# Performance work log

Hardware: AMD Instinct MI355X
Metric: run time of the kernel (lower is better)

Reference implementation:

```python
import jax, jax.numpy as jnp
import numpy as np

D = 32          # embedding_size
B = 16384       # batch_size
P = 16          # neighbor_sample_size (paths per item per hop)
NE = 100000     # n_entity
NU = 100000     # n_user
NR = 32         # n_relation
N_ITER = 2


def setup_inputs() -> dict:
    key = jax.random.key(0)
    ks = jax.random.split(key, 20)
    s = 0.1
    nrm = lambda k, sh: jax.random.normal(k, sh, dtype=jnp.float32) * s
    inp = {
        "user_table": nrm(ks[0], (NU, D)),
        "ent_table": nrm(ks[1], (NE, D)),
        "rel_table": nrm(ks[2], (NR, D)),
        # PyTorch LSTM params, gate order (i, f, g, o)
        "w_ih0": nrm(ks[3], (4 * D, 2 * D)),
        "w_hh0": nrm(ks[4], (4 * D, D)),
        "b_ih0": nrm(ks[5], (4 * D,)),
        "b_hh0": nrm(ks[6], (4 * D,)),
        "w_ih1": nrm(ks[7], (4 * D, 2 * D)),
        "w_hh1": nrm(ks[8], (4 * D, D)),
        "b_ih1": nrm(ks[9], (4 * D,)),
        "b_hh1": nrm(ks[10], (4 * D,)),
        "agg_w": nrm(ks[11], (D, D)),
        "agg_b": nrm(ks[12], (D,)),
        "users": jax.random.randint(ks[13], (B,), 0, NU),
        "items": jax.random.randint(ks[14], (B,), 0, NE),
        "ratings": jax.random.randint(ks[15], (B,), 0, 2),
        # hop h path table: [n_entity, P, 2*(h+1)+1]; values < 32 valid for both tables
        "lp0": jax.random.randint(ks[16], (NE, P, 3), 0, 32),
        "lp1": jax.random.randint(ks[17], (NE, P, 5), 0, 32),
    }
    return inp


def _lstm_last(seq, w_ih, w_hh, b_ih, b_hh):
    # seq: [N, T, 2D] -> final hidden state [N, D], PyTorch gate order i,f,g,o
    N = seq.shape[0]
    H = w_hh.shape[1]
    bias = b_ih + b_hh

    def step(carry, x):
        h, c = carry
        g = x @ w_ih.T + h @ w_hh.T + bias
        i, f, gg, o = jnp.split(g, 4, axis=-1)
        c = jax.nn.sigmoid(f) * c + jax.nn.sigmoid(i) * jnp.tanh(gg)
        h = jax.nn.sigmoid(o) * jnp.tanh(c)
        return (h, c), None

    h0 = jnp.zeros((N, H), seq.dtype)
    (h, _), _ = jax.lax.scan(step, (h0, h0), jnp.swapaxes(seq, 0, 1))
    return h


def _forward(user_table, ent_table, rel_table, lstm_params, agg_w, agg_b,
             users, items, ratings, lps):
    u = user_table[users]                # [B, D]
    items_emb = ent_table[items]         # [B, D]
    for hop in range(N_ITER):
        lp = lps[hop]
        w_ih, w_hh, b_ih, b_hh = lstm_params[hop]
        il = lp[items]                   # [B, P, 2*(hop+1)+1]
        seed_e = ent_table[il[:, :, 0]]  # [B, P, D]
        u_b = jnp.broadcast_to(u[:, None, :], seed_e.shape)
        first = jnp.concatenate([u_b, seed_e], -1)[:, :, None, :]   # [B,P,1,2D]
        rel_e = rel_table[il[:, :, 1::2]]                            # [B,P,hop+1,D]
        tail_e = ent_table[il[:, :, 2::2]]                           # [B,P,hop+1,D]
        rest = jnp.concatenate([rel_e, tail_e], -1)                  # [B,P,hop+1,2D]
        seq = jnp.concatenate([first, rest], 2).reshape(B * P, hop + 2, 2 * D)
        h = _lstm_last(seq, w_ih, w_hh, b_ih, b_hh)                  # [B*P, D]
        final = h.reshape(B, P, D).sum(axis=1)                       # hidden_out sum
        items_emb = (items_emb + final) @ agg_w.T + agg_b            # 'sum' aggregator
    scores = jnp.sum(u * items_emb, axis=-1)                         # [B]
    r = ratings.astype(scores.dtype)
    # stable BCE on sigmoid(scores)
    loss = -jnp.mean(r * jax.nn.log_sigmoid(scores) + (1.0 - r) * jax.nn.log_sigmoid(-scores))
    return loss, jax.nn.sigmoid(scores)


def reference(user_table, ent_table, rel_table,
              w_ih0, w_hh0, b_ih0, b_hh0,
              w_ih1, w_hh1, b_ih1, b_hh1,
              agg_w, agg_b,
              users, items, ratings, lp0, lp1):
    lstm_params = [(w_ih0, w_hh0, b_ih0, b_hh0), (w_ih1, w_hh1, b_ih1, b_hh1)]
    loss, scores_normalized = _forward(user_table, ent_table, rel_table,
                                       lstm_params, agg_w, agg_b,
                                       users, items, ratings, (lp0, lp1))
    return (loss, scores_normalized, items)
```

## Files before the change

### kernel.cpp

```cpp
#include <hip/hip_runtime.h>
#include <math.h>

#define D  32
#define BN 16384
#define PP 16

typedef __bf16 bf16x8 __attribute__((ext_vector_type(8)));
typedef __bf16 bf16x4 __attribute__((ext_vector_type(4)));
typedef float  floatx4 __attribute__((ext_vector_type(4)));

#define K1 1.44269504088896341f
#define K2 2.88539008177792681f

#define TR_OFF    0
#define TE_OFF    8448
#define BIAS_OFF  16896
#define WU_OFF    17408
#define WHH_OFF   27648
#define IMG_BYTES 37888
#define LDS_BYTES (IMG_BYTES + 8 * 1280)

__device__ __forceinline__ float sigf(float x) {
    float e = __builtin_amdgcn_exp2f(-x * K1);
    return __builtin_amdgcn_rcpf(1.0f + e);
}
__device__ __forceinline__ float logsigf(float x) {
    float ax = fabsf(x);
    float l = log1pf(__expf(-ax));
    return (x >= 0.0f) ? -l : x - l;
}
__device__ __forceinline__ floatx4 cvt4(bf16x4 v) {
    floatx4 r = { (float)v[0], (float)v[1], (float)v[2], (float)v[3] };
    return r;
}
__device__ __forceinline__ bf16x8 loadu8(const float* __restrict__ p) {
    float4 a = ((const float4*)p)[0], b = ((const float4*)p)[1];
    bf16x8 r = { (__bf16)a.x, (__bf16)a.y, (__bf16)a.z, (__bf16)a.w,
                 (__bf16)b.x, (__bf16)b.y, (__bf16)b.z, (__bf16)b.w };
    return r;
}

__global__ __launch_bounds__(256)
void prep_tables(const float* __restrict__ ent, const float* __restrict__ rel,
                 const float* __restrict__ wih0, const float* __restrict__ whh0,
                 const float* __restrict__ bih0, const float* __restrict__ bhh0,
                 const float* __restrict__ wih1, const float* __restrict__ whh1,
                 const float* __restrict__ bih1, const float* __restrict__ bhh1,
                 float* __restrict__ imgs_f)
{
    const int id = blockIdx.x * 256 + threadIdx.x;
    if (id < 16384) {
        const int hop = id >> 13;
        const int rest = id & 8191;
        const int tab = rest >> 12;
        const int k   = (rest >> 7) & 31;
        const int g   = rest & 127;
        const float* wih = hop ? wih1 : wih0;
        char* base = (char*)imgs_f + (size_t)hop * IMG_BYTES;
        if (tab == 0) {
            const float* w = wih + (size_t)g * 64;
            const float* s = rel + (size_t)k * 32;
            float a = (hop ? bih1[g] + bhh1[g] : bih0[g] + bhh0[g]);
            #pragma unroll
            for (int d = 0; d < 32; ++d) a = fmaf(w[d], s[d], a);
            *((__bf16*)(base + TR_OFF) + k * 132 + g) = (__bf16)a;
        } else {
            const float* w = wih + (size_t)g * 64 + 32;
            const float* s = ent + (size_t)k * 32;
            float a = 0.0f;
            #pragma unroll
            for (int d = 0; d < 32; ++d) a = fmaf(w[d], s[d], a);
            *((__bf16*)(base + TE_OFF) + k * 132 + g) = (__bf16)a;
        }
    } else if (id < 32768) {
        const int id2 = id - 16384;
        const int hop = id2 >> 13;
        const int rest = id2 & 8191;
        const int mat  = rest >> 12;
        const int e    = rest & 4095;
        const int gate = e >> 5, d = e & 31;
        char* base = (char*)imgs_f + (size_t)hop * IMG_BYTES;
        float v;
        if (mat == 0) v = (hop ? wih1 : wih0)[(size_t)gate * 64 + d];
        else          v = (hop ? whh1 : whh0)[(size_t)gate * 32 + d];
        *((__bf16*)(base + (mat ? WHH_OFF : WU_OFF)) + gate * 40 + d) = (__bf16)v;
    } else if (id < 33024) {
        const int id3 = id - 32768;
        const int hop = id3 >> 7;
        const int g   = id3 & 127;
        char* base = (char*)imgs_f + (size_t)hop * IMG_BYTES;
        ((float*)(base + BIAS_OFF))[g] = hop ? (bih1[g] + bhh1[g])
                                             : (bih0[g] + bhh0[g]);
    }
}

template<bool FIRST, bool LAST>
__device__ __forceinline__ void nonlin(
    floatx4* __restrict__ acc, float* __restrict__ cst,
    float* __restrict__ hlo, float* __restrict__ hhi,
    char* __restrict__ Hw, int q, int bnl)
{
    #pragma unroll
    for (int hf = 0; hf < 2; ++hf) {
        float* hout = hf ? hhi : hlo;
        #pragma unroll
        for (int r = 0; r < 4; ++r) {
            float gi = acc[0 + hf][r], gf = acc[2 + hf][r],
                  gg = acc[4 + hf][r], go = acc[6 + hf][r];
            float Ai = 1.0f + __builtin_amdgcn_exp2f(-gi * K1);
            float Af = 1.0f + __builtin_amdgcn_exp2f(-gf * K1);
            float G2 = __builtin_amdgcn_exp2f(gg * K2);
            float Gp = G2 + 1.0f, Gm = G2 - 1.0f;
            float cold = FIRST ? 0.0f : cst[hf * 4 + r];
            float num = cold * Ai * Gp + Gm * Af;
            float c = num * __builtin_amdgcn_rcpf(Af * Ai * Gp);
            cst[hf * 4 + r] = c;
            float Ao = 1.0f + __builtin_amdgcn_exp2f(-go * K1);
            float C2 = __builtin_amdgcn_exp2f(c * K2);
            hout[r] = (C2 - 1.0f) * __builtin_amdgcn_rcpf(Ao * (C2 + 1.0f));
        }
    }
    if (!LAST) {
        bf16x4 plo = { (__bf16)hlo[0], (__bf16)hlo[1], (__bf16)hlo[2], (__bf16)hlo[3] };
        bf16x4 phi = { (__bf16)hhi[0], (__bf16)hhi[1], (__bf16)hhi[2], (__bf16)hhi[3] };
        *(bf16x4*)(Hw + bnl * 80 + 8 * q)      = plo;
        *(bf16x4*)(Hw + bnl * 80 + 32 + 8 * q) = phi;
    }
}

__global__ __launch_bounds__(256, 3)
void hop_mfma(const float* __restrict__ user_table,
              const int*   __restrict__ users,
              const int*   __restrict__ items,
              const int*   __restrict__ lp0,
              const int*   __restrict__ lp1,
              const float* __restrict__ imgs_f,
              float* __restrict__ F0,
              float* __restrict__ F1)
{
    __shared__ __align__(16) char lds[LDS_BYTES];

    const bool second = blockIdx.x & 1;
    const int  idx    = blockIdx.x >> 1;
    const int tid  = threadIdx.x;
    const int lane = tid & 63;
    const int wave = tid >> 6;
    const int q    = lane >> 4;
    const int bnl  = lane & 15;

    {
        const float4* g = (const float4*)((const char*)imgs_f +
                                          (second ? IMG_BYTES : 0));
        float4* l = (float4*)lds;
        #pragma unroll
        for (int i = 0; i < 10; ++i) {
            int k = i * 256 + tid;
            if (k < IMG_BYTES / 16) l[k] = g[k];
        }
    }

    const char* Tr  = lds + TR_OFF;
    const char* Te  = lds + TE_OFF;
    const char* Wu  = lds + WU_OFF;
    const char* Whh = lds + WHH_OFF;
    char* HwA = lds + IMG_BYTES + (wave * 2 + 0) * 1280;
    char* HwB = lds + IMG_BYTES + (wave * 2 + 1) * 1280;

    const int fbA = idx * 8 + wave;
    const int fbB = fbA + 4;
    const int L   = second ? 5 : 3;
    const int* lp = second ? lp1 : lp0;
    const int* __restrict__ ilA = lp + ((size_t)items[fbA] * PP + bnl) * L;
    const int* __restrict__ ilB = lp + ((size_t)items[fbB] * PP + bnl) * L;

    bf16x8 buA = loadu8(user_table + (size_t)users[fbA] * D + q * 8);
    bf16x8 buB = loadu8(user_table + (size_t)users[fbB] * D + q * 8);

    __syncthreads();

    float cstA[8], cstB[8], hloA[4], hhiA[4], hloB[4], hhiB[4];

    {
        const int sA = ilA[0], sB = ilB[0];
        floatx4 accA[8], accB[8];
        #pragma unroll
        for (int mt = 0; mt < 8; ++mt) {
            const int go = 16 * mt + 4 * q;
            floatx4 bv = *(const floatx4*)(lds + BIAS_OFF + go * 4);
            accA[mt] = bv + cvt4(*(const bf16x4*)(Te + sA * 264 + go * 2));
            accB[mt] = bv + cvt4(*(const bf16x4*)(Te + sB * 264 + go * 2));
        }
        #pragma unroll
        for (int mt = 0; mt < 8; ++mt) {
            bf16x8 wu = *(const bf16x8*)(Wu + (16 * mt + bnl) * 80 + q * 16);
            accA[mt] = __builtin_amdgcn_mfma_f32_16x16x32_bf16(wu, buA, accA[mt], 0, 0, 0);
            accB[mt] = __builtin_amdgcn_mfma_f32_16x16x32_bf16(wu, buB, accB[mt], 0, 0, 0);
        }
        nonlin<true, false>(accA, cstA, hloA, hhiA, HwA, q, bnl);
        nonlin<true, false>(accB, cstB, hloB, hhiB, HwB, q, bnl);
    }

    #pragma unroll
    for (int t = 1; t < 3; ++t) {
        if (t == 2 && !second) break;
        const bool last = (t == (second ? 2 : 1));
        const int jA = ilA[2 * t - 1], kA = ilA[2 * t];
        const int jB = ilB[2 * t - 1], kB = ilB[2 * t];
        floatx4 accA[8], accB[8];
        #pragma unroll
        for (int mt = 0; mt < 8; ++mt) {
            const int go = 16 * mt + 4 * q;
            accA[mt] = cvt4(*(const bf16x4*)(Tr + jA * 264 + go * 2))
                     + cvt4(*(const bf16x4*)(Te + kA * 264 + go * 2));
            accB[mt] = cvt4(*(const bf16x4*)(Tr + jB * 264 + go * 2))
                     + cvt4(*(const bf16x4*)(Te + kB * 264 + go * 2));
        }
        bf16x8 bhA = *(const bf16x8*)(HwA + bnl * 80 + q * 16);
        bf16x8 bhB = *(const bf16x8*)(HwB + bnl * 80 + q * 16);
        #pragma unroll
        for (int mt = 0; mt < 8; ++mt) {
            bf16x8 wh = *(const bf16x8*)(Whh + (16 * mt + bnl) * 80 + q * 16);
            accA[mt] = __builtin_amdgcn_mfma_f32_16x16x32_bf16(wh, bhA, accA[mt], 0, 0, 0);
            accB[mt] = __builtin_amdgcn_mfma_f32_16x16x32_bf16(wh, bhB, accB[mt], 0, 0, 0);
        }
        if (last) {
            nonlin<false, true>(accA, cstA, hloA, hhiA, HwA, q, bnl);
            nonlin<false, true>(accB, cstB, hloB, hhiB, HwB, q, bnl);
        } else {
            nonlin<false, false>(accA, cstA, hloA, hhiA, HwA, q, bnl);
            nonlin<false, false>(accB, cstB, hloB, hhiB, HwB, q, bnl);
        }
    }

    #pragma unroll
    for (int r = 0; r < 4; ++r) {
        #pragma unroll
        for (int m = 1; m < 16; m <<= 1) {
            hloA[r] += __shfl_xor(hloA[r], m);
            hhiA[r] += __shfl_xor(hhiA[r], m);
            hloB[r] += __shfl_xor(hloB[r], m);
            hhiB[r] += __shfl_xor(hhiB[r], m);
        }
    }
    if (bnl == 0) {
        float* Fout = (second ? F1 : F0);
        float4 vloA = { hloA[0], hloA[1], hloA[2], hloA[3] };
        float4 vhiA = { hhiA[0], hhiA[1], hhiA[2], hhiA[3] };
        float4 vloB = { hloB[0], hloB[1], hloB[2], hloB[3] };
        float4 vhiB = { hhiB[0], hhiB[1], hhiB[2], hhiB[3] };
        *(float4*)(Fout + (size_t)fbA * D + 4 * q)      = vloA;
        *(float4*)(Fout + (size_t)fbA * D + 16 + 4 * q) = vhiA;
        *(float4*)(Fout + (size_t)fbB * D + 4 * q)      = vloB;
        *(float4*)(Fout + (size_t)fbB * D + 16 + 4 * q) = vhiB;
    }
}

__global__ __launch_bounds__(256)
void chain_score(const float* __restrict__ user_table,
                 const float* __restrict__ ent_table,
                 const float* __restrict__ agg_w,
                 const float* __restrict__ agg_b,
                 const int*   __restrict__ users,
                 const int*   __restrict__ items,
                 const int*   __restrict__ ratings,
                 const float* __restrict__ F0,
                 const float* __restrict__ F1,
                 float* __restrict__ out,
                 float* __restrict__ partials)
{
    __shared__ float s[8][33];
    __shared__ float red[8];
    const int tid = threadIdx.x;
    const int bb  = tid >> 5;
    const int j   = tid & 31;
    const int b   = blockIdx.x * 8 + bb;
    const int it  = items[b];

    s[bb][j] = ent_table[(size_t)it * D + j] + F0[(size_t)b * D + j];
    __syncthreads();
    const float* __restrict__ w = agg_w + (size_t)j * D;
    float e0 = agg_b[j];
    #pragma unroll
    for (int k = 0; k < D; ++k) e0 = fmaf(s[bb][k], w[k], e0);
    __syncthreads();
    s[bb][j] = e0 + F1[(size_t)b * D + j];
    __syncthreads();
    float e1 = agg_b[j];
    #pragma unroll
    for (int k = 0; k < D; ++k) e1 = fmaf(s[bb][k], w[k], e1);

    float prod = user_table[(size_t)users[b] * D + j] * e1;
    #pragma unroll
    for (int m = 1; m < 32; m <<= 1) prod += __shfl_xor(prod, m);
    if (j == 0) {
        out[1 + b]      = sigf(prod);
        out[1 + BN + b] = (float)it;
        float r = (float)ratings[b];
        red[bb] = r * logsigf(prod) + (1.0f - r) * logsigf(-prod);
    }
    __syncthreads();
    if (tid == 0) {
        float t = 0.0f;
        #pragma unroll
        for (int qq = 0; qq < 8; ++qq) t += red[qq];
        partials[blockIdx.x] = t;
    }
}

__global__ __launch_bounds__(256)
void loss_kernel(const float* __restrict__ partials, float* __restrict__ out)
{
    __shared__ float red[4];
    const int t = threadIdx.x;
    float v = 0.0f;
    #pragma unroll
    for (int qq = 0; qq < 8; ++qq) v += partials[qq * 256 + t];
    #pragma unroll
    for (int m = 1; m < 64; m <<= 1) v += __shfl_xor(v, m);
    if ((t & 63) == 0) red[t >> 6] = v;
    __syncthreads();
    if (t == 0) out[0] = -(red[0] + red[1] + red[2] + red[3]) / (float)BN;
}

extern "C" void kernel_launch(void* const* d_in, const int* in_sizes, int n_in,
                              void* d_out, int out_size, void* d_ws, size_t ws_size,
                              hipStream_t stream)
{
    const float* user_table = (const float*)d_in[0];
    const float* ent_table  = (const float*)d_in[1];
    const float* rel_table  = (const float*)d_in[2];
    const float* w_ih0 = (const float*)d_in[3];
    const float* w_hh0 = (const float*)d_in[4];
    const float* b_ih0 = (const float*)d_in[5];
    const float* b_hh0 = (const float*)d_in[6];
    const float* w_ih1 = (const float*)d_in[7];
    const float* w_hh1 = (const float*)d_in[8];
    const float* b_ih1 = (const float*)d_in[9];
    const float* b_hh1 = (const float*)d_in[10];
    const float* agg_w = (const float*)d_in[11];
    const float* agg_b = (const float*)d_in[12];
    const int* users   = (const int*)d_in[13];
    const int* items   = (const int*)d_in[14];
    const int* ratings = (const int*)d_in[15];
    const int* lp0     = (const int*)d_in[16];
    const int* lp1     = (const int*)d_in[17];
    float* out = (float*)d_out;

    float* ws       = (float*)d_ws;
    float* F0       = ws;
    float* F1       = ws + (size_t)BN * D;
    float* partials = ws + 2 * (size_t)BN * D;
    float* imgs     = ws + 2 * (size_t)BN * D + 2048;

    prep_tables<<<130, 256, 0, stream>>>(ent_table, rel_table,
        w_ih0, w_hh0, b_ih0, b_hh0, w_ih1, w_hh1, b_ih1, b_hh1, imgs);
    hop_mfma<<<4096, 256, 0, stream>>>(
        user_table, users, items, lp0, lp1, imgs, F0, F1);
    chain_score<<<BN / 8, 256, 0, stream>>>(
        user_table, ent_table, agg_w, agg_b, users, items, ratings,
        F0, F1, out, partials);
    loss_kernel<<<1, 256, 0, stream>>>(partials, out);
}
```

Before: 232.4 us.

## Replace LDS table gathers with one-hot MFMA lookups and register-resident Wu

The precomputed relation/entity gate tables are now stored transposed, and per-path lookups are done as one-hot MFMA products instead of scattered bf16x4 LDS gathers plus conversions. The bias is folded into the entity table, the Wu weights are held in registers loaded straight from global memory, and LDS padding is shrunk. With the smaller LDS footprint the launch bound rises to 4 blocks per CU. This trades divergent LDS reads and cvt ALU work for extra MFMA instructions and more register pressure.

```diff
diff --git a/kernel.cpp b/kernel.cpp
--- a/kernel.cpp
+++ b/kernel.cpp
@@ -12,13 +12,13 @@
 #define K1 1.44269504088896341f
 #define K2 2.88539008177792681f
 
-#define TR_OFF    0
-#define TE_OFF    8448
-#define BIAS_OFF  16896
-#define WU_OFF    17408
-#define WHH_OFF   27648
-#define IMG_BYTES 37888
-#define LDS_BYTES (IMG_BYTES + 8 * 1280)
+#define WHH_OFF   0
+#define TR_OFF    8704
+#define TE_OFF    17408
+#define LDS_IMG   26112
+#define WU_OFF    26112
+#define IMG_BYTES 34304
+#define LDS_BYTES (LDS_IMG + 8 * 1152)
 
 __device__ __forceinline__ float sigf(float x) {
     float e = __builtin_amdgcn_exp2f(-x * K1);
@@ -29,14 +29,17 @@
     float l = log1pf(__expf(-ax));
     return (x >= 0.0f) ? -l : x - l;
 }
-__device__ __forceinline__ floatx4 cvt4(bf16x4 v) {
-    floatx4 r = { (float)v[0], (float)v[1], (float)v[2], (float)v[3] };
-    return r;
-}
 __device__ __forceinline__ bf16x8 loadu8(const float* __restrict__ p) {
     float4 a = ((const float4*)p)[0], b = ((const float4*)p)[1];
     bf16x8 r = { (__bf16)a.x, (__bf16)a.y, (__bf16)a.z, (__bf16)a.w,
                  (__bf16)b.x, (__bf16)b.y, (__bf16)b.z, (__bf16)b.w };
+    return r;
+}
+__device__ __forceinline__ bf16x8 onehot(int j, int q) {
+    bf16x8 r;
+    #pragma unroll
+    for (int i = 0; i < 8; ++i)
+        r[i] = (8 * q + i == j) ? (__bf16)1.0f : (__bf16)0.0f;
     return r;
 }
 
@@ -60,19 +63,19 @@
         if (tab == 0) {
             const float* w = wih + (size_t)g * 64;
             const float* s = rel + (size_t)k * 32;
-            float a = (hop ? bih1[g] + bhh1[g] : bih0[g] + bhh0[g]);
+            float a = 0.0f;
             #pragma unroll
             for (int d = 0; d < 32; ++d) a = fmaf(w[d], s[d], a);
-            *((__bf16*)(base + TR_OFF) + k * 132 + g) = (__bf16)a;
+            *((__bf16*)(base + TR_OFF) + g * 34 + k) = (__bf16)a;
         } else {
             const float* w = wih + (size_t)g * 64 + 32;
             const float* s = ent + (size_t)k * 32;
-            float a = 0.0f;
+            float a = hop ? (bih1[g] + bhh1[g]) : (bih0[g] + bhh0[g]);
             #pragma unroll
             for (int d = 0; d < 32; ++d) a = fmaf(w[d], s[d], a);
-            *((__bf16*)(base + TE_OFF) + k * 132 + g) = (__bf16)a;
-        }
-    } else if (id < 32768) {
+            *((__bf16*)(base + TE_OFF) + g * 34 + k) = (__bf16)a;
+        }
+    } else {
         const int id2 = id - 16384;
         const int hop = id2 >> 13;
         const int rest = id2 & 8191;
@@ -80,17 +83,13 @@
         const int e    = rest & 4095;
         const int gate = e >> 5, d = e & 31;
         char* base = (char*)imgs_f + (size_t)hop * IMG_BYTES;
-        float v;
-        if (mat == 0) v = (hop ? wih1 : wih0)[(size_t)gate * 64 + d];
-        else          v = (hop ? whh1 : whh0)[(size_t)gate * 32 + d];
-        *((__bf16*)(base + (mat ? WHH_OFF : WU_OFF)) + gate * 40 + d) = (__bf16)v;
-    } else if (id < 33024) {
-        const int id3 = id - 32768;
-        const int hop = id3 >> 7;
-        const int g   = id3 & 127;
-        char* base = (char*)imgs_f + (size_t)hop * IMG_BYTES;
-        ((float*)(base + BIAS_OFF))[g] = hop ? (bih1[g] + bhh1[g])
-                                             : (bih0[g] + bhh0[g]);
+        if (mat == 0) {
+            float v = (hop ? wih1 : wih0)[(size_t)gate * 64 + d];
+            *((__bf16*)(base + WU_OFF) + gate * 32 + d) = (__bf16)v;
+        } else {
+            float v = (hop ? whh1 : whh0)[(size_t)gate * 32 + d];
+            *((__bf16*)(base + WHH_OFF) + gate * 34 + d) = (__bf16)v;
+        }
     }
 }
 
@@ -123,12 +122,12 @@
     if (!LAST) {
         bf16x4 plo = { (__bf16)hlo[0], (__bf16)hlo[1], (__bf16)hlo[2], (__bf16)hlo[3] };
         bf16x4 phi = { (__bf16)hhi[0], (__bf16)hhi[1], (__bf16)hhi[2], (__bf16)hhi[3] };
-        *(bf16x4*)(Hw + bnl * 80 + 8 * q)      = plo;
-        *(bf16x4*)(Hw + bnl * 80 + 32 + 8 * q) = phi;
-    }
-}
-
-__global__ __launch_bounds__(256, 3)
+        *(bf16x4*)(Hw + bnl * 72 + 8 * q)      = plo;
+        *(bf16x4*)(Hw + bnl * 72 + 32 + 8 * q) = phi;
+    }
+}
+
+__global__ __launch_bounds__(256, 4)
 void hop_mfma(const float* __restrict__ user_table,
               const int*   __restrict__ users,
               const int*   __restrict__ items,
@@ -148,23 +147,25 @@
     const int q    = lane >> 4;
     const int bnl  = lane & 15;
 
+    const char* imgG = (const char*)imgs_f + (second ? IMG_BYTES : 0);
+
     {
-        const float4* g = (const float4*)((const char*)imgs_f +
-                                          (second ? IMG_BYTES : 0));
+        const float4* g = (const float4*)imgG;
         float4* l = (float4*)lds;
         #pragma unroll
-        for (int i = 0; i < 10; ++i) {
+        for (int i = 0; i < 7; ++i) {
             int k = i * 256 + tid;
-            if (k < IMG_BYTES / 16) l[k] = g[k];
-        }
-    }
-
-    const char* Tr  = lds + TR_OFF;
-    const char* Te  = lds + TE_OFF;
-    const char* Wu  = lds + WU_OFF;
-    const char* Whh = lds + WHH_OFF;
-    char* HwA = lds + IMG_BYTES + (wave * 2 + 0) * 1280;
-    char* HwB = lds + IMG_BYTES + (wave * 2 + 1) * 1280;
+            if (k < LDS_IMG / 16) l[k] = g[k];
+        }
+    }
+
+    bf16x8 WuF[8];
+    {
+        const __bf16* wu = (const __bf16*)(imgG + WU_OFF);
+        #pragma unroll
+        for (int mt = 0; mt < 8; ++mt)
+            WuF[mt] = *(const bf16x8*)(wu + (16 * mt + bnl) * 32 + q * 8);
+    }
 
     const int fbA = idx * 8 + wave;
     const int fbB = fbA + 4;
@@ -178,23 +179,26 @@
 
     __syncthreads();
 
+    const char* Whh = lds + WHH_OFF;
+    const char* Tr  = lds + TR_OFF;
+    const char* Te  = lds + TE_OFF;
+    char* HwA = lds + LDS_IMG + (wave * 2 + 0) * 1152;
+    char* HwB = lds + LDS_IMG + (wave * 2 + 1) * 1152;
+
     float cstA[8], cstB[8], hloA[4], hhiA[4], hloB[4], hhiB[4];
 
     {
-        const int sA = ilA[0], sB = ilB[0];
+        bf16x8 ohA = onehot(ilA[0], q);
+        bf16x8 ohB = onehot(ilB[0], q);
         floatx4 accA[8], accB[8];
         #pragma unroll
         for (int mt = 0; mt < 8; ++mt) {
-            const int go = 16 * mt + 4 * q;
-            floatx4 bv = *(const floatx4*)(lds + BIAS_OFF + go * 4);
-            accA[mt] = bv + cvt4(*(const bf16x4*)(Te + sA * 264 + go * 2));
-            accB[mt] = bv + cvt4(*(const bf16x4*)(Te + sB * 264 + go * 2));
-        }
-        #pragma unroll
-        for (int mt = 0; mt < 8; ++mt) {
-            bf16x8 wu = *(const bf16x8*)(Wu + (16 * mt + bnl) * 80 + q * 16);
-            accA[mt] = __builtin_amdgcn_mfma_f32_16x16x32_bf16(wu, buA, accA[mt], 0, 0, 0);
-            accB[mt] = __builtin_amdgcn_mfma_f32_16x16x32_bf16(wu, buB, accB[mt], 0, 0, 0);
+            bf16x8 teF = *(const bf16x8*)(Te + (16 * mt + bnl) * 68 + q * 16);
+            floatx4 z = { 0.f, 0.f, 0.f, 0.f };
+            accA[mt] = __builtin_amdgcn_mfma_f32_16x16x32_bf16(teF, ohA, z, 0, 0, 0);
+            accB[mt] = __builtin_amdgcn_mfma_f32_16x16x32_bf16(teF, ohB, z, 0, 0, 0);
+            accA[mt] = __builtin_amdgcn_mfma_f32_16x16x32_bf16(WuF[mt], buA, accA[mt], 0, 0, 0);
+            accB[mt] = __builtin_amdgcn_mfma_f32_16x16x32_bf16(WuF[mt], buB, accB[mt], 0, 0, 0);
         }
         nonlin<true, false>(accA, cstA, hloA, hhiA, HwA, q, bnl);
         nonlin<true, false>(accB, cstB, hloB, hhiB, HwB, q, bnl);
@@ -204,24 +208,28 @@
     for (int t = 1; t < 3; ++t) {
         if (t == 2 && !second) break;
         const bool last = (t == (second ? 2 : 1));
-        const int jA = ilA[2 * t - 1], kA = ilA[2 * t];
-        const int jB = ilB[2 * t - 1], kB = ilB[2 * t];
+        bf16x8 ojA = onehot(ilA[2 * t - 1], q);
+        bf16x8 okA = onehot(ilA[2 * t], q);
+        bf16x8 ojB = onehot(ilB[2 * t - 1], q);
+        bf16x8 okB = onehot(ilB[2 * t], q);
+        bf16x8 bhA = *(const bf16x8*)(HwA + bnl * 72 + q * 16);
+        bf16x8 bhB = *(const bf16x8*)(HwB + bnl * 72 + q * 16);
         floatx4 accA[8], accB[8];
         #pragma unroll
         for (int mt = 0; mt < 8; ++mt) {
-            const int go = 16 * mt + 4 * q;
-            accA[mt] = cvt4(*(const bf16x4*)(Tr + jA * 264 + go * 2))
-                     + cvt4(*(const bf16x4*)(Te + kA * 264 + go * 2));
-            accB[mt] = cvt4(*(const bf16x4*)(Tr + jB * 264 + go * 2))
-                     + cvt4(*(const bf16x4*)(Te + kB * 264 + go * 2));
-        }
-        bf16x8 bhA = *(const bf16x8*)(HwA + bnl * 80 + q * 16);
-        bf16x8 bhB = *(const bf16x8*)(HwB + bnl * 80 + q * 16);
-        #pragma unroll
-        for (int mt = 0; mt < 8; ++mt) {
-            bf16x8 wh = *(const bf16x8*)(Whh + (16 * mt + bnl) * 80 + q * 16);
-            accA[mt] = __builtin_amdgcn_mfma_f32_16x16x32_bf16(wh, bhA, accA[mt], 0, 0, 0);
-            accB[mt] = __builtin_amdgcn_mfma_f32_16x16x32_bf16(wh, bhB, accB[mt], 0, 0, 0);
+            const int ro = (16 * mt + bnl) * 68 + q * 16;
+            bf16x8 trF = *(const bf16x8*)(Tr + ro);
+            bf16x8 teF = *(const bf16x8*)(Te + ro);
+            bf16x8 whF = *(const bf16x8*)(Whh + ro);
+            floatx4 z = { 0.f, 0.f, 0.f, 0.f };
+            floatx4 a = __builtin_amdgcn_mfma_f32_16x16x32_bf16(trF, ojA, z, 0, 0, 0);
+            floatx4 b = __builtin_amdgcn_mfma_f32_16x16x32_bf16(trF, ojB, z, 0, 0, 0);
+            a = __builtin_amdgcn_mfma_f32_16x16x32_bf16(teF, okA, a, 0, 0, 0);
+            b = __builtin_amdgcn_mfma_f32_16x16x32_bf16(teF, okB, b, 0, 0, 0);
+            a = __builtin_amdgcn_mfma_f32_16x16x32_bf16(whF, bhA, a, 0, 0, 0);
+            b = __builtin_amdgcn_mfma_f32_16x16x32_bf16(whF, bhB, b, 0, 0, 0);
+            accA[mt] = a;
+            accB[mt] = b;
         }
         if (last) {
             nonlin<false, true>(accA, cstA, hloA, hhiA, HwA, q, bnl);
@@ -352,7 +360,7 @@
     float* partials = ws + 2 * (size_t)BN * D;
     float* imgs     = ws + 2 * (size_t)BN * D + 2048;
 
-    prep_tables<<<130, 256, 0, stream>>>(ent_table, rel_table,
+    prep_tables<<<128, 256, 0, stream>>>(ent_table, rel_table,
         w_ih0, w_hh0, b_ih0, b_hh0, w_ih1, w_hh1, b_ih1, b_hh1, imgs);
     hop_mfma<<<4096, 256, 0, stream>>>(
         user_table, users, items, lp0, lp1, imgs, F0, F1);
```

After: 286.1 us. 23.1% more time.
